# Performance work log

Measured on AMD Instinct MI355X. Metric: run time of the kernel, lower is better.

## Reference

```python
import jax, jax.numpy as jnp
import numpy as np

N = 10000       # nodes (= number of eigenpairs)
NFEAT = 512
NCLASS = 64     # hidden size of attention/FFN when norm='none'
HID = 128       # feat_encoder hidden
DIM = 32        # eig encoder hidden_dim
K = 10          # outer loop count of ParamNonHarmonicEncoding
NF = DIM // 2   # num_freq = 16
OMEGA = 50.0
DMIN = 0.25
NLAYER = 1


def _ln(x, g, b, eps=1e-5):
    m = jnp.mean(x, axis=-1, keepdims=True)
    v = jnp.mean((x - m) ** 2, axis=-1, keepdims=True)
    return g * (x - m) / jnp.sqrt(v + eps) + b


def setup_inputs() -> dict:
    key = jax.random.key(0)
    ks = jax.random.split(key, 32)
    f32 = jnp.float32
    def w(k, shape, s=0.05):
        return jax.random.normal(k, shape, dtype=f32) * s
    inp = {
        "e": jax.random.uniform(ks[0], (N,), dtype=f32),
        "u": jax.random.normal(ks[1], (N, N), dtype=f32) / np.float32(np.sqrt(N)),
        "x": jax.random.normal(ks[2], (N, NFEAT), dtype=f32),
        # feat_encoder: Linear(nfeat,hid) -> ReLU -> Linear(hid,nclass)
        "fe_w1": w(ks[3], (NFEAT, HID)), "fe_b1": jnp.zeros((HID,), f32),
        "fe_w2": w(ks[4], (HID, NCLASS)), "fe_b2": jnp.zeros((NCLASS,), f32),
        # ParamNonHarmonicEncoding
        "freq_deltas": jax.random.uniform(ks[5], (NF,), dtype=f32) * 0.5,
        "freq_bias": jnp.zeros((), f32),
        "readout_w": w(ks[6], (K, 1 + 2 * NF), 0.1),
        "readout_b": jnp.zeros((K,), f32),
        "alpha_w": w(ks[7], (K, 1), 0.3),   # nn.Linear(k,1,bias=False)
        # mha pre-norm
        "mha_ln_g": jnp.ones((NCLASS,), f32), "mha_ln_b": jnp.zeros((NCLASS,), f32),
        # Diff attention (H=1, hidden=nclass)
        "wq1": w(ks[8], (NCLASS, NCLASS)), "bq1": jnp.zeros((NCLASS,), f32),
        "wk1": w(ks[9], (NCLASS, NCLASS)), "bk1": jnp.zeros((NCLASS,), f32),
        "wq2": w(ks[10], (NCLASS, NCLASS)), "bq2": jnp.zeros((NCLASS,), f32),
        "wk2": w(ks[11], (NCLASS, NCLASS)), "bk2": jnp.zeros((NCLASS,), f32),
        "wv": w(ks[12], (NCLASS, NCLASS)), "bv": jnp.zeros((NCLASS,), f32),
        "lq1": w(ks[13], (NCLASS,), 0.1), "lk1": w(ks[14], (NCLASS,), 0.1),
        "lq2": w(ks[15], (NCLASS,), 0.1), "lk2": w(ks[16], (NCLASS,), 0.1),
        "attn_ln_g": jnp.ones((NCLASS,), f32), "attn_ln_b": jnp.zeros((NCLASS,), f32),
        "out_w": w(ks[17], (NCLASS, NCLASS)), "out_b": jnp.zeros((NCLASS,), f32),
        # gating
        "gate_ln_g": jnp.ones((3 * NCLASS,), f32), "gate_ln_b": jnp.zeros((3 * NCLASS,), f32),
        "gate_w": w(ks[18], (3 * NCLASS, 3)), "gate_b": jnp.zeros((3,), f32),
        # FFN
        "ffn_ln_g": jnp.ones((NCLASS,), f32), "ffn_ln_b": jnp.zeros((NCLASS,), f32),
        "ffn_w1": w(ks[19], (NCLASS, NCLASS)), "ffn_b1": jnp.zeros((NCLASS,), f32),
        "ffn_w2": w(ks[20], (NCLASS, NCLASS)), "ffn_b2": jnp.zeros((NCLASS,), f32),
    }
    return inp


def reference(e, u, x, fe_w1, fe_b1, fe_w2, fe_b2,
              freq_deltas, freq_bias, readout_w, readout_b, alpha_w,
              mha_ln_g, mha_ln_b,
              wq1, bq1, wk1, bk1, wq2, bq2, wk2, bk2, wv, bv,
              lq1, lk1, lq2, lk2, attn_ln_g, attn_ln_b, out_w, out_b,
              gate_ln_g, gate_ln_b, gate_w, gate_b,
              ffn_ln_g, ffn_ln_b, ffn_w1, ffn_b1, ffn_w2, ffn_b2):
    # feat encoder (all dropouts are 0 / eval mode)
    h = jnp.maximum(x @ fe_w1 + fe_b1, 0.0) @ fe_w2 + fe_b2          # [N, C]

    # ParamNonHarmonicEncoding, vectorized over the k powers
    deltas = jax.nn.softplus(freq_deltas) + DMIN
    freqs = jnp.cumsum(deltas) + freq_bias
    freqs = OMEGA * jnp.tanh(freqs / OMEGA)                           # [F]
    powers = e[:, None] ** jnp.arange(1, K + 1, dtype=e.dtype)        # [N, K]
    phase = powers[:, :, None] * freqs                                # [N, K, F]
    ns = jnp.asarray(NF ** 0.5, e.dtype)
    feat = jnp.concatenate(
        [jnp.ones_like(powers)[..., None], jnp.sin(phase) / ns, jnp.cos(phase) / ns],
        axis=-1)                                                      # [N, K, 1+2F]
    eig = jnp.einsum('nkf,kf->nk', feat, readout_w) + readout_b      # [N, K]
    new_e = eig @ alpha_w                                             # [N, 1]

    for layer in range(NLAYER):
        # spectral propagation: u @ diag-like(new_e) @ u^T @ h
        utx = u.T @ h                                                 # [N, C]
        h_fur = u @ (new_e * utx)                                     # [N, C]

        # differential linear attention
        mh = _ln(h, mha_ln_g, mha_ln_b)
        q1 = mh @ wq1 + bq1; k1 = mh @ wk1 + bk1
        q2 = mh @ wq2 + bq2; k2 = mh @ wk2 + bk2
        v = mh @ wv + bv
        k1v = k1.T @ v                                                # [C, C]
        k2v = k2.T @ v
        lam1 = jnp.exp(jnp.sum(lq1 * lk1))
        lam2 = jnp.exp(jnp.sum(lq2 * lk2))
        lam_init = 0.8 - 0.6 * float(np.exp(-0.3 * layer))
        lam_full = lam1 - lam2 + lam_init
        xa = q1 @ k1v - (q2 @ k2v) * lam_full
        xa = _ln(xa, attn_ln_g, attn_ln_b) * (1.0 - lam_init)
        mha_h = xa @ out_w + out_b                                    # [N, C]

        # gated mixing
        cat = jnp.concatenate([h, mha_h, h_fur], axis=-1)             # [N, 3C]
        g = jax.nn.softmax(_ln(cat, gate_ln_g, gate_ln_b) @ gate_w + gate_b, axis=-1)
        mix = h * g[:, 0:1] + mha_h * g[:, 1:2] + h_fur * g[:, 2:3]

        f = _ln(mix, ffn_ln_g, ffn_ln_b)
        f = jax.nn.gelu(f @ ffn_w1 + ffn_b1, approximate=False) @ ffn_w2 + ffn_b2
        h = mix + f
    return h
```

## Files before the change

kernel.cpp:

```cpp
#include <hip/hip_runtime.h>
#include <hip/hip_bf16.h>
#include <math.h>

#define NN 10000
#define J48 10048
#define CHUNKS 157
#define CPS 10
#define SPLITS 16

typedef __bf16 bf16;
typedef bf16 bf16x8 __attribute__((ext_vector_type(8)));
typedef float f32x4 __attribute__((ext_vector_type(4)));

__device__ __forceinline__ float wave_sum64(float v) {
#pragma unroll
  for (int m = 32; m >= 1; m >>= 1) v += __shfl_xor(v, m, 64);
  return v;
}

__global__ void prep_kernel(const float* __restrict__ w1, const float* __restrict__ w2,
                            const float* __restrict__ wq1, const float* __restrict__ wk1,
                            const float* __restrict__ wq2, const float* __restrict__ wk2,
                            const float* __restrict__ wvw,
                            const float* __restrict__ bq1, const float* __restrict__ bk1,
                            const float* __restrict__ bq2, const float* __restrict__ bk2,
                            const float* __restrict__ bvv,
                            const float* __restrict__ lq1, const float* __restrict__ lk1,
                            const float* __restrict__ lq2, const float* __restrict__ lk2,
                            const float* __restrict__ freq_deltas, const float* __restrict__ freq_bias,
                            bf16* __restrict__ w1T, bf16* __restrict__ w2T, bf16* __restrict__ qkvT,
                            float* __restrict__ bqkv, float* __restrict__ freqs, float* __restrict__ lamb) {
  int tid = blockIdx.x * blockDim.x + threadIdx.x;
  int nthr = gridDim.x * blockDim.x;
  for (int i = tid; i < 512 * 128; i += nthr) {
    int o = i >> 9, k = i & 511;
    w1T[i] = (bf16)w1[k * 128 + o];
  }
  for (int i = tid; i < 64 * 128; i += nthr) {
    int o = i >> 7, k = i & 127;
    w2T[i] = (bf16)w2[k * 64 + o];
  }
  for (int i = tid; i < 320 * 64; i += nthr) {
    int r = i >> 6, k = i & 63;
    const float* W = (r < 64) ? wq1 : (r < 128) ? wk1 : (r < 192) ? wq2 : (r < 256) ? wk2 : wvw;
    qkvT[i] = (bf16)W[k * 64 + (r & 63)];
  }
  for (int i = tid; i < 320; i += nthr) {
    const float* B = (i < 64) ? bq1 : (i < 128) ? bk1 : (i < 192) ? bq2 : (i < 256) ? bk2 : bvv;
    bqkv[i] = B[i & 63];
  }
  if (blockIdx.x == 0) {
    if (threadIdx.x == 0) {
      float acc = freq_bias[0];
      for (int f = 0; f < 16; f++) {
        acc += log1pf(expf(freq_deltas[f])) + 0.25f;
        freqs[f] = 50.0f * tanhf(acc * (1.0f / 50.0f));
      }
    }
    if (threadIdx.x >= 64 && threadIdx.x < 128) {
      int l = threadIdx.x - 64;
      float s1 = wave_sum64(lq1[l] * lk1[l]);
      float s2 = wave_sum64(lq2[l] * lk2[l]);
      if (l == 0) lamb[0] = expf(s1) - expf(s2) + 0.2f;
    }
  }
}

__global__ void newe_kernel(const float* __restrict__ e, const float* __restrict__ rw,
                            const float* __restrict__ rb, const float* __restrict__ aw,
                            const float* __restrict__ freqs, float* __restrict__ newe) {
  int n = blockIdx.x * blockDim.x + threadIdx.x;
  if (n >= NN) return;
  float fr[16];
#pragma unroll
  for (int f = 0; f < 16; f++) fr[f] = freqs[f];
  float ev = e[n], p = 1.0f, acc = 0.0f;
  for (int k = 0; k < 10; k++) {
    p *= ev;
    float s = rb[k] + rw[k * 33];
#pragma unroll
    for (int f = 0; f < 16; f++) {
      float ph = p * fr[f];
      s += 0.25f * (__sinf(ph) * rw[k * 33 + 1 + f] + __cosf(ph) * rw[k * 33 + 17 + f]);
    }
    acc += s * aw[k];
  }
  newe[n] = acc;
}

__global__ __launch_bounds__(256) void g1_kernel(const float* __restrict__ x, const bf16* __restrict__ w1T,
                                                 const float* __restrict__ b1, bf16* __restrict__ t1b) {
  __shared__ bf16 la[64][40];
  __shared__ bf16 lb[128][40];
  const int bm = blockIdx.x * 64;
  const int lane = threadIdx.x & 63, wvid = threadIdx.x >> 6;
  const int am = threadIdx.x >> 2, aseg = (threadIdx.x & 3) * 8;
  const int arow = bm + am;
  f32x4 acc[8] = {};
  float4 aLo, aHi;
  uint4 bChunk[2];
  auto fetchAll = [&](int k0) {
    if (arow < NN) {
      const float4* p = (const float4*)(x + (size_t)arow * 512 + k0 + aseg);
      aLo = p[0]; aHi = p[1];
    } else {
      aLo = make_float4(0.f, 0.f, 0.f, 0.f); aHi = aLo;
    }
#pragma unroll
    for (int r = 0; r < 2; r++) {
      int slot = threadIdx.x * 2 + r;
      int n = slot >> 2, seg = (slot & 3) * 8;
      bChunk[r] = *(const uint4*)(w1T + n * 512 + k0 + seg);
    }
  };
  auto store = [&]() {
    union { uint4 v; bf16 b[8]; } pk;
    float av[8] = {aLo.x, aLo.y, aLo.z, aLo.w, aHi.x, aHi.y, aHi.z, aHi.w};
#pragma unroll
    for (int t = 0; t < 8; t++) pk.b[t] = (bf16)av[t];
    *(uint4*)&la[am][aseg] = pk.v;
#pragma unroll
    for (int r = 0; r < 2; r++) {
      int slot = threadIdx.x * 2 + r;
      int n = slot >> 2, seg = (slot & 3) * 8;
      *(uint4*)&lb[n][seg] = bChunk[r];
    }
  };
  fetchAll(0);
  for (int k0 = 0; k0 < 512; k0 += 32) {
    store();
    if (k0 + 32 < 512) fetchAll(k0 + 32);
    __syncthreads();
    bf16x8 af = *(const bf16x8*)&la[wvid * 16 + (lane & 15)][(lane >> 4) * 8];
#pragma unroll
    for (int s = 0; s < 8; s++) {
      bf16x8 bfr = *(const bf16x8*)&lb[s * 16 + (lane & 15)][(lane >> 4) * 8];
      acc[s] = __builtin_amdgcn_mfma_f32_16x16x32_bf16(af, bfr, acc[s], 0, 0, 0);
    }
    __syncthreads();
  }
#pragma unroll
  for (int s = 0; s < 8; s++) {
    int col = s * 16 + (lane & 15);
    float bvv = b1[col];
#pragma unroll
    for (int r = 0; r < 4; r++) {
      int row = bm + wvid * 16 + (lane >> 4) * 4 + r;
      if (row < NN) {
        float v = acc[s][r] + bvv;
        t1b[(size_t)row * 128 + col] = (bf16)(v > 0.f ? v : 0.f);
      }
    }
  }
}

__global__ __launch_bounds__(256) void g2_kernel(const bf16* __restrict__ t1b, const bf16* __restrict__ w2T,
                                                 const float* __restrict__ b2, float* __restrict__ h,
                                                 bf16* __restrict__ hT) {
  __shared__ bf16 la[64][72];
  __shared__ bf16 lb[64][72];
  const int bm = blockIdx.x * 64;
  const int lane = threadIdx.x & 63, wvid = threadIdx.x >> 6;
  f32x4 acc[4] = {};
  for (int k0 = 0; k0 < 128; k0 += 64) {
#pragma unroll
    for (int r = 0; r < 2; r++) {
      int slot = threadIdx.x * 2 + r;
      int m = slot >> 3, seg = (slot & 7) * 8;
      int row = bm + m;
      uint4 val = make_uint4(0u, 0u, 0u, 0u);
      if (row < NN) val = *(const uint4*)(t1b + (size_t)row * 128 + k0 + seg);
      *(uint4*)&la[m][seg] = val;
      *(uint4*)&lb[m][seg] = *(const uint4*)(w2T + m * 128 + k0 + seg);
    }
    __syncthreads();
#pragma unroll
    for (int ks = 0; ks < 2; ks++) {
      bf16x8 af = *(const bf16x8*)&la[wvid * 16 + (lane & 15)][ks * 32 + (lane >> 4) * 8];
#pragma unroll
      for (int s = 0; s < 4; s++) {
        bf16x8 bfr = *(const bf16x8*)&lb[s * 16 + (lane & 15)][ks * 32 + (lane >> 4) * 8];
        acc[s] = __builtin_amdgcn_mfma_f32_16x16x32_bf16(af, bfr, acc[s], 0, 0, 0);
      }
    }
    __syncthreads();
  }
#pragma unroll
  for (int s = 0; s < 4; s++) {
    int col = s * 16 + (lane & 15);
    float bvv = b2[col];
#pragma unroll
    for (int r = 0; r < 4; r++) {
      int row = bm + wvid * 16 + (lane >> 4) * 4 + r;
      if (row < NN) {
        float v = acc[s][r] + bvv;
        h[(size_t)row * 64 + col] = v;
        hT[(size_t)col * NN + row] = (bf16)v;
      }
    }
  }
}

__global__ __launch_bounds__(256) void mhln_kernel(const float* __restrict__ h, const float* __restrict__ g,
                                                   const float* __restrict__ b, bf16* __restrict__ mh) {
  int row = blockIdx.x * 4 + (threadIdx.x >> 6);
  int lane = threadIdx.x & 63;
  if (row >= NN) return;
  float v = h[(size_t)row * 64 + lane];
  float m = wave_sum64(v) * (1.0f / 64.0f);
  float d = v - m;
  float var = wave_sum64(d * d) * (1.0f / 64.0f);
  mh[(size_t)row * 64 + lane] = (bf16)(g[lane] * d * rsqrtf(var + 1e-5f) + b[lane]);
}

__global__ __launch_bounds__(256) void qkv_kernel(const bf16* __restrict__ mh, const bf16* __restrict__ qkvT,
                                                  const float* __restrict__ bqkv,
                                                  bf16* __restrict__ qq, bf16* __restrict__ kv) {
  __shared__ bf16 la[64][72];
  __shared__ bf16 lb[320][72];
  const int bm = blockIdx.x * 64;
  const int lane = threadIdx.x & 63, wvid = threadIdx.x >> 6;
#pragma unroll
  for (int r = 0; r < 2; r++) {
    int slot = threadIdx.x * 2 + r;
    int m = slot >> 3, seg = (slot & 7) * 8;
    int row = bm + m;
    uint4 val = make_uint4(0u, 0u, 0u, 0u);
    if (row < NN) val = *(const uint4*)(mh + (size_t)row * 64 + seg);
    *(uint4*)&la[m][seg] = val;
  }
#pragma unroll
  for (int r = 0; r < 10; r++) {
    int slot = threadIdx.x * 10 + r;
    int n = slot >> 3, seg = (slot & 7) * 8;
    *(uint4*)&lb[n][seg] = *(const uint4*)(qkvT + n * 64 + seg);
  }
  __syncthreads();
  f32x4 acc[20] = {};
#pragma unroll
  for (int ks = 0; ks < 2; ks++) {
    bf16x8 af = *(const bf16x8*)&la[wvid * 16 + (lane & 15)][ks * 32 + (lane >> 4) * 8];
#pragma unroll
    for (int s = 0; s < 20; s++) {
      bf16x8 bfr = *(const bf16x8*)&lb[s * 16 + (lane & 15)][ks * 32 + (lane >> 4) * 8];
      acc[s] = __builtin_amdgcn_mfma_f32_16x16x32_bf16(af, bfr, acc[s], 0, 0, 0);
    }
  }
#pragma unroll
  for (int s = 0; s < 20; s++) {
    int col = s * 16 + (lane & 15);
    float bvv = bqkv[col];
    bf16* dst; int dc, stride;
    if (col < 64)       { dst = qq; dc = col;       stride = 128; }
    else if (col < 128) { dst = kv; dc = col - 64;  stride = 192; }
    else if (col < 192) { dst = qq; dc = col - 64;  stride = 128; }
    else                { dst = kv; dc = col - 128; stride = 192; }
#pragma unroll
    for (int r = 0; r < 4; r++) {
      int row = bm + wvid * 16 + (lane >> 4) * 4 + r;
      if (row < NN) dst[(size_t)row * stride + dc] = (bf16)(acc[s][r] + bvv);
    }
  }
}

__global__ __launch_bounds__(256) void r1_kernel(const bf16* __restrict__ kv, float* __restrict__ part) {
  int b = blockIdx.x;
  int c1 = threadIdx.x & 63, grp = threadIdx.x >> 6;
  int r0 = b * 40;
  float a1[16] = {}, a2[16] = {};
  for (int r = 0; r < 40; r++) {
    const bf16* rowp = kv + (size_t)(r0 + r) * 192;
    float k1 = (float)rowp[c1];
    float k2 = (float)rowp[64 + c1];
#pragma unroll
    for (int q = 0; q < 16; q++) {
      float vv = (float)rowp[128 + grp * 16 + q];
      a1[q] += k1 * vv; a2[q] += k2 * vv;
    }
  }
  float* p1 = part + ((size_t)(b * 2 + 0) * 64 + c1) * 64 + grp * 16;
  float* p2 = part + ((size_t)(b * 2 + 1) * 64 + c1) * 64 + grp * 16;
#pragma unroll
  for (int q = 0; q < 16; q++) { p1[q] = a1[q]; p2[q] = a2[q]; }
}

__global__ __launch_bounds__(256) void r2a_kernel(const float* __restrict__ part, float* __restrict__ part2) {
  int flat = blockIdx.x * 256 + threadIdx.x;
  int y = blockIdx.y;
  int b0 = y * 32, b1 = min(250, b0 + 32);
  float s = 0.f;
  for (int b = b0; b < b1; b++) s += part[(size_t)b * 8192 + flat];
  part2[(size_t)flat * 8 + y] = s;
}

__global__ void r2b_kernel(const float* __restrict__ part2, const float* __restrict__ lamb, bf16* __restrict__ Bt) {
  int flat = blockIdx.x * 256 + threadIdx.x;
  int mat = flat >> 12, rem = flat & 4095;
  int d = rem >> 6, c = rem & 63;
  f32x4 lo = *(const f32x4*)(part2 + (size_t)flat * 8);
  f32x4 hi = *(const f32x4*)(part2 + (size_t)flat * 8 + 4);
  float s = lo[0] + lo[1] + lo[2] + lo[3] + hi[0] + hi[1] + hi[2] + hi[3];
  float v = mat ? (-lamb[0] * s) : s;
  Bt[c * 128 + mat * 64 + d] = (bf16)v;
}

__global__ __launch_bounds__(256) void d_split_kernel(const float* __restrict__ u, const bf16* __restrict__ hT,
                                                      float* __restrict__ dpart) {
  __shared__ bf16 la[64][72];
  __shared__ bf16 lb[64][72];
  const int j0 = blockIdx.x * 64;
  const int sk = blockIdx.y;
  const int c0 = sk * CPS, c1e = min(CHUNKS, c0 + CPS);
  const int t = threadIdx.x;
  const int lane = t & 63, wv = t >> 6;
  const int jl = (t & 15) * 4;
  const int ir = (t >> 4) * 4;
  f32x4 acc[4] = {};
  uint4 aC[2];
  float4 bC[4];
  auto fetchAll = [&](int i0) {
#pragma unroll
    for (int r = 0; r < 2; r++) {
      int slot = t * 2 + r;
      int c = slot >> 3, seg = (slot & 7) * 8;
      int i = i0 + seg;
      if (i + 7 < NN) aC[r] = *(const uint4*)(hT + (size_t)c * NN + i);
      else {
        union { uint4 v; bf16 b[8]; } tu;
#pragma unroll
        for (int q = 0; q < 8; q++) tu.b[q] = (i + q < NN) ? hT[(size_t)c * NN + i + q] : (bf16)0.f;
        aC[r] = tu.v;
      }
    }
#pragma unroll
    for (int q = 0; q < 4; q++) {
      int i = i0 + ir + q;
      if (i < NN && (j0 + jl + 3) < NN) bC[q] = *(const float4*)(u + (size_t)i * NN + j0 + jl);
      else if (i < NN) {
        float tmp[4];
#pragma unroll
        for (int q2 = 0; q2 < 4; q2++) tmp[q2] = (j0 + jl + q2 < NN) ? u[(size_t)i * NN + j0 + jl + q2] : 0.f;
        bC[q] = make_float4(tmp[0], tmp[1], tmp[2], tmp[3]);
      } else bC[q] = make_float4(0.f, 0.f, 0.f, 0.f);
    }
  };
  auto storeAll = [&]() {
#pragma unroll
    for (int r = 0; r < 2; r++) {
      int slot = t * 2 + r;
      int c = slot >> 3, seg = (slot & 7) * 8;
      *(uint4*)&la[c][seg] = aC[r];
    }
#pragma unroll
    for (int q2 = 0; q2 < 4; q2++) {
      int j = jl + q2;
      int isw = ir ^ (((j >> 2) & 3) << 3);
      union { uint2 w; bf16 b[4]; } pk;
      pk.b[0] = (bf16)((float*)&bC[0])[q2];
      pk.b[1] = (bf16)((float*)&bC[1])[q2];
      pk.b[2] = (bf16)((float*)&bC[2])[q2];
      pk.b[3] = (bf16)((float*)&bC[3])[q2];
      *(uint2*)&lb[j][isw] = pk.w;
    }
  };
  fetchAll(c0 * 64);
  for (int ch = c0; ch < c1e; ch++) {
    storeAll();
    if (ch + 1 < c1e) fetchAll((ch + 1) * 64);
    __syncthreads();
#pragma unroll
    for (int ks = 0; ks < 2; ks++) {
      bf16x8 af = *(const bf16x8*)&la[wv * 16 + (lane & 15)][ks * 32 + (lane >> 4) * 8];
#pragma unroll
      for (int s = 0; s < 4; s++) {
        int j = s * 16 + (lane & 15);
        int ioff = (ks * 32 + (lane >> 4) * 8) ^ (((j >> 2) & 3) << 3);
        bf16x8 bfr = *(const bf16x8*)&lb[j][ioff];
        acc[s] = __builtin_amdgcn_mfma_f32_16x16x32_bf16(af, bfr, acc[s], 0, 0, 0);
      }
    }
    __syncthreads();
  }
#pragma unroll
  for (int s = 0; s < 4; s++) {
    int col = s * 16 + (lane & 15);
#pragma unroll
    for (int r = 0; r < 4; r++) {
      int c = wv * 16 + (lane >> 4) * 4 + r;
      dpart[((size_t)sk * 64 + c) * J48 + j0 + col] = acc[s][r];
    }
  }
}

__global__ void dred_kernel(const float* __restrict__ dpart, const float* __restrict__ newe,
                            bf16* __restrict__ wutxT) {
  int idx = blockIdx.x * 256 + threadIdx.x;
  int c = idx / 2512;
  int j = (idx - c * 2512) * 4;
  if (c >= 64 || j >= NN) return;
  f32x4 s = {};
  for (int sk = 0; sk < SPLITS; sk++)
    s += *(const f32x4*)(dpart + ((size_t)sk * 64 + c) * J48 + j);
  union { uint2 w; bf16 b[4]; } pk;
#pragma unroll
  for (int q = 0; q < 4; q++) pk.b[q] = (bf16)(newe[j + q] * s[q]);
  *(uint2*)&wutxT[(size_t)c * NN + j] = pk.w;
}

__global__ __launch_bounds__(256) void e_split_kernel(const float* __restrict__ u, const bf16* __restrict__ wutxT,
                                                      float* __restrict__ epart) {
  __shared__ bf16 la[64][72];
  __shared__ bf16 lb[64][72];
  const int bm = blockIdx.x * 64;
  const int sk = blockIdx.y;
  const int c0 = sk * CPS, c1e = min(CHUNKS, c0 + CPS);
  const int t = threadIdx.x;
  const int lane = t & 63, wv = t >> 6;
  const int mA = t >> 2, segA = (t & 3) * 16;
  const int mrow = bm + mA;
  f32x4 acc[4] = {};
  float4 aC[4];
  uint4 bC[2];
  auto fetchAll = [&](int j0) {
    int j = j0 + segA;
    if (mrow < NN && j + 15 < NN) {
      const float4* p = (const float4*)(u + (size_t)mrow * NN + j);
      aC[0] = p[0]; aC[1] = p[1]; aC[2] = p[2]; aC[3] = p[3];
    } else {
#pragma unroll
      for (int q = 0; q < 4; q++) {
        float tmp[4];
#pragma unroll
        for (int q2 = 0; q2 < 4; q2++) {
          int jj = j + q * 4 + q2;
          tmp[q2] = (mrow < NN && jj < NN) ? u[(size_t)mrow * NN + jj] : 0.f;
        }
        aC[q] = make_float4(tmp[0], tmp[1], tmp[2], tmp[3]);
      }
    }
#pragma unroll
    for (int r = 0; r < 2; r++) {
      int slot = t * 2 + r;
      int c = slot >> 3, seg = (slot & 7) * 8;
      int jj = j0 + seg;
      if (jj + 7 < NN) bC[r] = *(const uint4*)(wutxT + (size_t)c * NN + jj);
      else {
        union { uint4 v; bf16 b[8]; } tu;
#pragma unroll
        for (int q = 0; q < 8; q++) tu.b[q] = (jj + q < NN) ? wutxT[(size_t)c * NN + jj + q] : (bf16)0.f;
        bC[r] = tu.v;
      }
    }
  };
  auto storeAll = [&]() {
    union { uint4 v[2]; bf16 b[16]; } pk;
#pragma unroll
    for (int q = 0; q < 4; q++)
#pragma unroll
      for (int q2 = 0; q2 < 4; q2++) pk.b[q * 4 + q2] = (bf16)((float*)&aC[q])[q2];
    *(uint4*)&la[mA][segA] = pk.v[0];
    *(uint4*)&la[mA][segA + 8] = pk.v[1];
#pragma unroll
    for (int r = 0; r < 2; r++) {
      int slot = t * 2 + r;
      int c = slot >> 3, seg = (slot & 7) * 8;
      *(uint4*)&lb[c][seg] = bC[r];
    }
  };
  fetchAll(c0 * 64);
  for (int ch = c0; ch < c1e; ch++) {
    storeAll();
    if (ch + 1 < c1e) fetchAll((ch + 1) * 64);
    __syncthreads();
#pragma unroll
    for (int ks = 0; ks < 2; ks++) {
      bf16x8 af = *(const bf16x8*)&la[wv * 16 + (lane & 15)][ks * 32 + (lane >> 4) * 8];
#pragma unroll
      for (int s = 0; s < 4; s++) {
        bf16x8 bfr = *(const bf16x8*)&lb[s * 16 + (lane & 15)][ks * 32 + (lane >> 4) * 8];
        acc[s] = __builtin_amdgcn_mfma_f32_16x16x32_bf16(af, bfr, acc[s], 0, 0, 0);
      }
    }
    __syncthreads();
  }
#pragma unroll
  for (int s = 0; s < 4; s++) {
    int col = s * 16 + (lane & 15);
#pragma unroll
    for (int r = 0; r < 4; r++) {
      int row = wv * 16 + (lane >> 4) * 4 + r;
      epart[((size_t)sk * J48 + bm + row) * 64 + col] = acc[s][r];
    }
  }
}

__global__ void ered_kernel(const float* __restrict__ epart, float* __restrict__ h_fur) {
  int idx = blockIdx.x * 256 + threadIdx.x;
  if (idx >= NN * 16) return;
  size_t off = (size_t)idx * 4;
  f32x4 s = {};
  for (int sk = 0; sk < SPLITS; sk++)
    s += *(const f32x4*)(epart + (size_t)sk * (J48 * 64) + off);
  *(f32x4*)(h_fur + off) = s;
}

__global__ __launch_bounds__(256) void hattn_kernel(const bf16* __restrict__ qq, const bf16* __restrict__ Bt,
                                                    const float* __restrict__ g, const float* __restrict__ b,
                                                    bf16* __restrict__ xan) {
  __shared__ bf16 la[64][136];
  __shared__ bf16 lb[64][136];
  const int bm = blockIdx.x * 64;
  const int lane = threadIdx.x & 63, wvid = threadIdx.x >> 6;
#pragma unroll
  for (int r = 0; r < 4; r++) {
    int slot = threadIdx.x * 4 + r;
    int m = slot >> 4, seg = (slot & 15) * 8;
    int row = bm + m;
    uint4 val = make_uint4(0u, 0u, 0u, 0u);
    if (row < NN) val = *(const uint4*)(qq + (size_t)row * 128 + seg);
    *(uint4*)&la[m][seg] = val;
    *(uint4*)&lb[m][seg] = *(const uint4*)(Bt + m * 128 + seg);
  }
  __syncthreads();
  f32x4 acc[4] = {};
#pragma unroll
  for (int ks = 0; ks < 4; ks++) {
    bf16x8 af = *(const bf16x8*)&la[wvid * 16 + (lane & 15)][ks * 32 + (lane >> 4) * 8];
#pragma unroll
    for (int s = 0; s < 4; s++) {
      bf16x8 bfr = *(const bf16x8*)&lb[s * 16 + (lane & 15)][ks * 32 + (lane >> 4) * 8];
      acc[s] = __builtin_amdgcn_mfma_f32_16x16x32_bf16(af, bfr, acc[s], 0, 0, 0);
    }
  }
#pragma unroll
  for (int r = 0; r < 4; r++) {
    float psum = acc[0][r] + acc[1][r] + acc[2][r] + acc[3][r];
#pragma unroll
    for (int msk = 1; msk < 16; msk <<= 1) psum += __shfl_xor(psum, msk, 64);
    float mean = psum * (1.0f / 64.0f);
    float pvar = 0.f;
#pragma unroll
    for (int s = 0; s < 4; s++) { float dd = acc[s][r] - mean; pvar += dd * dd; }
#pragma unroll
    for (int msk = 1; msk < 16; msk <<= 1) pvar += __shfl_xor(pvar, msk, 64);
    float rsq = rsqrtf(pvar * (1.0f / 64.0f) + 1e-5f);
    int row = bm + wvid * 16 + (lane >> 4) * 4 + r;
    if (row < NN) {
#pragma unroll
      for (int s = 0; s < 4; s++) {
        int col = s * 16 + (lane & 15);
        float o = 0.8f * (g[col] * (acc[s][r] - mean) * rsq + b[col]);
        xan[(size_t)row * 64 + col] = (bf16)o;
      }
    }
  }
}

__global__ __launch_bounds__(256) void final_kernel(const float* __restrict__ h, const float* __restrict__ h_fur,
                                                    const bf16* __restrict__ xan,
                                                    const float* __restrict__ out_w, const float* __restrict__ out_b,
                                                    const float* __restrict__ gg, const float* __restrict__ gb,
                                                    const float* __restrict__ gw, const float* __restrict__ gbias,
                                                    const float* __restrict__ fg, const float* __restrict__ fb,
                                                    const float* __restrict__ fw1, const float* __restrict__ fb1,
                                                    const float* __restrict__ fw2, const float* __restrict__ fb2,
                                                    float* __restrict__ out) {
  __shared__ float s_ow[64][64];
  __shared__ float s_w1[64][64];
  __shared__ float s_w2[64][64];
  __shared__ float s_gw[192][3];
  __shared__ float s_row[4][64];
  const int lane = threadIdx.x & 63, wvid = threadIdx.x >> 6;
  for (int i = threadIdx.x; i < 4096; i += 256) {
    ((float*)s_ow)[i] = out_w[i];
    ((float*)s_w1)[i] = fw1[i];
    ((float*)s_w2)[i] = fw2[i];
  }
  for (int i = threadIdx.x; i < 576; i += 256) ((float*)s_gw)[i] = gw[i];
  const int row = blockIdx.x * 4 + wvid;
  float x_h = h[(size_t)row * 64 + lane];
  float x_f = h_fur[(size_t)row * 64 + lane];
  float x_a = (float)xan[(size_t)row * 64 + lane];
  s_row[wvid][lane] = x_a;
  __syncthreads();
  float mha = out_b[lane];
#pragma unroll 8
  for (int d = 0; d < 64; d++) mha += s_row[wvid][d] * s_ow[d][lane];
  float m3 = wave_sum64(x_h + mha + x_f) * (1.0f / 192.0f);
  float dh = x_h - m3, dm = mha - m3, df = x_f - m3;
  float v3 = wave_sum64(dh * dh + dm * dm + df * df) * (1.0f / 192.0f);
  float rs3 = rsqrtf(v3 + 1e-5f);
  float l0 = gg[lane] * dh * rs3 + gb[lane];
  float l1 = gg[64 + lane] * dm * rs3 + gb[64 + lane];
  float l2 = gg[128 + lane] * df * rs3 + gb[128 + lane];
  float p0 = l0 * s_gw[lane][0] + l1 * s_gw[64 + lane][0] + l2 * s_gw[128 + lane][0];
  float p1 = l0 * s_gw[lane][1] + l1 * s_gw[64 + lane][1] + l2 * s_gw[128 + lane][1];
  float p2 = l0 * s_gw[lane][2] + l1 * s_gw[64 + lane][2] + l2 * s_gw[128 + lane][2];
  p0 = wave_sum64(p0) + gbias[0];
  p1 = wave_sum64(p1) + gbias[1];
  p2 = wave_sum64(p2) + gbias[2];
  float mx = fmaxf(p0, fmaxf(p1, p2));
  float e0 = expf(p0 - mx), e1 = expf(p1 - mx), e2 = expf(p2 - mx);
  float inv = 1.0f / (e0 + e1 + e2);
  float mix = x_h * (e0 * inv) + mha * (e1 * inv) + x_f * (e2 * inv);
  float mf = wave_sum64(mix) * (1.0f / 64.0f);
  float dmx = mix - mf;
  float vf = wave_sum64(dmx * dmx) * (1.0f / 64.0f);
  float f = fg[lane] * dmx * rsqrtf(vf + 1e-5f) + fb[lane];
  __syncthreads();
  s_row[wvid][lane] = f;
  __syncthreads();
  float t1 = fb1[lane];
#pragma unroll 8
  for (int d = 0; d < 64; d++) t1 += s_row[wvid][d] * s_w1[d][lane];
  t1 = 0.5f * t1 * (1.0f + erff(t1 * 0.70710678118654752f));
  __syncthreads();
  s_row[wvid][lane] = t1;
  __syncthreads();
  float f2 = fb2[lane];
#pragma unroll 8
  for (int d = 0; d < 64; d++) f2 += s_row[wvid][d] * s_w2[d][lane];
  out[(size_t)row * 64 + lane] = mix + f2;
}

extern "C" void kernel_launch(void* const* d_in, const int* in_sizes, int n_in,
                              void* d_out, int out_size, void* d_ws, size_t ws_size,
                              hipStream_t stream) {
  const float* e          = (const float*)d_in[0];
  const float* u          = (const float*)d_in[1];
  const float* x          = (const float*)d_in[2];
  const float* fe_w1      = (const float*)d_in[3];
  const float* fe_b1      = (const float*)d_in[4];
  const float* fe_w2      = (const float*)d_in[5];
  const float* fe_b2      = (const float*)d_in[6];
  const float* freq_deltas= (const float*)d_in[7];
  const float* freq_bias  = (const float*)d_in[8];
  const float* readout_w  = (const float*)d_in[9];
  const float* readout_b  = (const float*)d_in[10];
  const float* alpha_w    = (const float*)d_in[11];
  const float* mha_ln_g   = (const float*)d_in[12];
  const float* mha_ln_b   = (const float*)d_in[13];
  const float* wq1        = (const float*)d_in[14];
  const float* bq1        = (const float*)d_in[15];
  const float* wk1        = (const float*)d_in[16];
  const float* bk1        = (const float*)d_in[17];
  const float* wq2        = (const float*)d_in[18];
  const float* bq2        = (const float*)d_in[19];
  const float* wk2        = (const float*)d_in[20];
  const float* bk2        = (const float*)d_in[21];
  const float* wv_in      = (const float*)d_in[22];
  const float* bv_in      = (const float*)d_in[23];
  const float* lq1        = (const float*)d_in[24];
  const float* lk1        = (const float*)d_in[25];
  const float* lq2        = (const float*)d_in[26];
  const float* lk2        = (const float*)d_in[27];
  const float* attn_ln_g  = (const float*)d_in[28];
  const float* attn_ln_b  = (const float*)d_in[29];
  const float* out_w      = (const float*)d_in[30];
  const float* out_b      = (const float*)d_in[31];
  const float* gate_ln_g  = (const float*)d_in[32];
  const float* gate_ln_b  = (const float*)d_in[33];
  const float* gate_w     = (const float*)d_in[34];
  const float* gate_b     = (const float*)d_in[35];
  const float* ffn_ln_g   = (const float*)d_in[36];
  const float* ffn_ln_b   = (const float*)d_in[37];
  const float* ffn_w1     = (const float*)d_in[38];
  const float* ffn_b1     = (const float*)d_in[39];
  const float* ffn_w2     = (const float*)d_in[40];
  const float* ffn_b2     = (const float*)d_in[41];

  constexpr size_t OFF_H     = 0;
  constexpr size_t OFF_T1B   = 2560000;
  constexpr size_t OFF_HT    = 5120000;
  constexpr size_t OFF_MH    = 6400000;
  constexpr size_t OFF_QQ    = 7680000;
  constexpr size_t OFF_KV    = 10240000;
  constexpr size_t OFF_WUTXT = 14080000;
  constexpr size_t OFF_HFUR  = 15360000;
  constexpr size_t OFF_XAN   = 17920000;
  constexpr size_t OFF_NEWE  = 19200000;
  constexpr size_t OFF_BT    = 19240064;
  constexpr size_t OFF_W1T   = 19256448;
  constexpr size_t OFF_W2T   = 19387520;
  constexpr size_t OFF_QKVT  = 19403904;
  constexpr size_t OFF_BQKV  = 19444864;
  constexpr size_t OFF_FREQS = 19446144;
  constexpr size_t OFF_LAM   = 19446208;
  constexpr size_t OFF_BIG   = 19446272;
  constexpr size_t OFF_PART2 = OFF_BIG + 8192000;
  constexpr size_t WS_NEED   = OFF_BIG + (size_t)SPLITS * J48 * 64 * 4;
  if (ws_size < WS_NEED) return;

  char* ws = (char*)d_ws;
  float* h_buf   = (float*)(ws + OFF_H);
  bf16*  t1b     = (bf16*)(ws + OFF_T1B);
  bf16*  hT      = (bf16*)(ws + OFF_HT);
  bf16*  mh      = (bf16*)(ws + OFF_MH);
  bf16*  qq      = (bf16*)(ws + OFF_QQ);
  bf16*  kv      = (bf16*)(ws + OFF_KV);
  bf16*  wutxT   = (bf16*)(ws + OFF_WUTXT);
  float* h_fur   = (float*)(ws + OFF_HFUR);
  bf16*  xan     = (bf16*)(ws + OFF_XAN);
  float* newe    = (float*)(ws + OFF_NEWE);
  bf16*  Bt      = (bf16*)(ws + OFF_BT);
  bf16*  w1T     = (bf16*)(ws + OFF_W1T);
  bf16*  w2T     = (bf16*)(ws + OFF_W2T);
  bf16*  qkvT    = (bf16*)(ws + OFF_QKVT);
  float* bqkv    = (float*)(ws + OFF_BQKV);
  float* freqs   = (float*)(ws + OFF_FREQS);
  float* lamb    = (float*)(ws + OFF_LAM);
  float* part    = (float*)(ws + OFF_BIG);
  float* part2   = (float*)(ws + OFF_PART2);
  float* spart   = (float*)(ws + OFF_BIG);

  prep_kernel<<<64, 256, 0, stream>>>(fe_w1, fe_w2, wq1, wk1, wq2, wk2, wv_in,
                                      bq1, bk1, bq2, bk2, bv_in,
                                      lq1, lk1, lq2, lk2, freq_deltas, freq_bias,
                                      w1T, w2T, qkvT, bqkv, freqs, lamb);
  newe_kernel<<<40, 256, 0, stream>>>(e, readout_w, readout_b, alpha_w, freqs, newe);
  g1_kernel<<<157, 256, 0, stream>>>(x, w1T, fe_b1, t1b);
  g2_kernel<<<157, 256, 0, stream>>>(t1b, w2T, fe_b2, h_buf, hT);
  mhln_kernel<<<2500, 256, 0, stream>>>(h_buf, mha_ln_g, mha_ln_b, mh);
  qkv_kernel<<<157, 256, 0, stream>>>(mh, qkvT, bqkv, qq, kv);
  r1_kernel<<<250, 256, 0, stream>>>(kv, part);
  r2a_kernel<<<dim3(32, 8), 256, 0, stream>>>(part, part2);
  r2b_kernel<<<32, 256, 0, stream>>>(part2, lamb, Bt);
  d_split_kernel<<<dim3(157, SPLITS), 256, 0, stream>>>(u, hT, spart);
  dred_kernel<<<628, 256, 0, stream>>>(spart, newe, wutxT);
  e_split_kernel<<<dim3(157, SPLITS), 256, 0, stream>>>(u, wutxT, spart);
  ered_kernel<<<625, 256, 0, stream>>>(spart, h_fur);
  hattn_kernel<<<157, 256, 0, stream>>>(qq, Bt, attn_ln_g, attn_ln_b, xan);
  final_kernel<<<2500, 256, 0, stream>>>(h_buf, h_fur, xan, out_w, out_b,
                                         gate_ln_g, gate_ln_b, gate_w, gate_b,
                                         ffn_ln_g, ffn_ln_b, ffn_w1, ffn_b1, ffn_w2, ffn_b2,
                                         (float*)d_out);
}
```

Measured before the change: 366.2 us.

## Pre-convert eigenvector matrix to bf16, fuse pre-norm LayerNorm into g2, retune splits

Adds a kernel that converts the 10000x10000 fp32 eigenvector matrix to bf16 once per call. Both spectral GEMMs (d_split and e_split) then stream half-size bf16 tiles and skip per-tile fp32-to-bf16 conversion. The aim is to cut the bytes those two large GEMMs read, at the cost of an extra full read of the fp32 matrix plus a 200MB bf16 write. It also fuses the MHA pre-LayerNorm into the g2 epilogue, which removes the mhln kernel. Other changes: r1 gets vectorized loads over more, smaller blocks, and the K-split count drops from 16 to 8 with twice as many chunks per split.

```diff
diff --git a/kernel.cpp b/kernel.cpp
--- a/kernel.cpp
+++ b/kernel.cpp
@@ -5,8 +5,8 @@
 #define NN 10000
 #define J48 10048
 #define CHUNKS 157
-#define CPS 10
-#define SPLITS 16
+#define CPS 20
+#define SPLITS 8
 
 typedef __bf16 bf16;
 typedef bf16 bf16x8 __attribute__((ext_vector_type(8)));
@@ -88,6 +88,19 @@
   newe[n] = acc;
 }
 
+__global__ __launch_bounds__(256) void ucopy_kernel(const float* __restrict__ u, bf16* __restrict__ ubf) {
+  size_t base = ((size_t)blockIdx.x * 256 + threadIdx.x) * 8;
+  size_t stride = (size_t)gridDim.x * 256 * 8;
+  for (size_t i = base; i < (size_t)NN * NN; i += stride) {
+    float4 a = *(const float4*)(u + i);
+    float4 b = *(const float4*)(u + i + 4);
+    union { uint4 v; bf16 h[8]; } pk;
+    pk.h[0] = (bf16)a.x; pk.h[1] = (bf16)a.y; pk.h[2] = (bf16)a.z; pk.h[3] = (bf16)a.w;
+    pk.h[4] = (bf16)b.x; pk.h[5] = (bf16)b.y; pk.h[6] = (bf16)b.z; pk.h[7] = (bf16)b.w;
+    *(uint4*)(ubf + i) = pk.v;
+  }
+}
+
 __global__ __launch_bounds__(256) void g1_kernel(const float* __restrict__ x, const bf16* __restrict__ w1T,
                                                  const float* __restrict__ b1, bf16* __restrict__ t1b) {
   __shared__ bf16 la[64][40];
@@ -155,8 +168,9 @@
 }
 
 __global__ __launch_bounds__(256) void g2_kernel(const bf16* __restrict__ t1b, const bf16* __restrict__ w2T,
-                                                 const float* __restrict__ b2, float* __restrict__ h,
-                                                 bf16* __restrict__ hT) {
+                                                 const float* __restrict__ b2, const float* __restrict__ lng,
+                                                 const float* __restrict__ lnb, float* __restrict__ h,
+                                                 bf16* __restrict__ hT, bf16* __restrict__ mh) {
   __shared__ bf16 la[64][72];
   __shared__ bf16 lb[64][72];
   const int bm = blockIdx.x * 64;
@@ -185,32 +199,38 @@
     }
     __syncthreads();
   }
+  float bv4[4], g4[4], lb4[4];
 #pragma unroll
   for (int s = 0; s < 4; s++) {
     int col = s * 16 + (lane & 15);
-    float bvv = b2[col];
-#pragma unroll
-    for (int r = 0; r < 4; r++) {
-      int row = bm + wvid * 16 + (lane >> 4) * 4 + r;
-      if (row < NN) {
-        float v = acc[s][r] + bvv;
+    bv4[s] = b2[col]; g4[s] = lng[col]; lb4[s] = lnb[col];
+  }
+#pragma unroll
+  for (int r = 0; r < 4; r++) {
+    float vals[4], psum = 0.f;
+#pragma unroll
+    for (int s = 0; s < 4; s++) { vals[s] = acc[s][r] + bv4[s]; psum += vals[s]; }
+#pragma unroll
+    for (int msk = 1; msk < 16; msk <<= 1) psum += __shfl_xor(psum, msk, 64);
+    float mean = psum * (1.0f / 64.0f);
+    float pvar = 0.f;
+#pragma unroll
+    for (int s = 0; s < 4; s++) { float dd = vals[s] - mean; pvar += dd * dd; }
+#pragma unroll
+    for (int msk = 1; msk < 16; msk <<= 1) pvar += __shfl_xor(pvar, msk, 64);
+    float rsq = rsqrtf(pvar * (1.0f / 64.0f) + 1e-5f);
+    int row = bm + wvid * 16 + (lane >> 4) * 4 + r;
+    if (row < NN) {
+#pragma unroll
+      for (int s = 0; s < 4; s++) {
+        int col = s * 16 + (lane & 15);
+        float v = vals[s];
         h[(size_t)row * 64 + col] = v;
         hT[(size_t)col * NN + row] = (bf16)v;
-      }
-    }
-  }
-}
-
-__global__ __launch_bounds__(256) void mhln_kernel(const float* __restrict__ h, const float* __restrict__ g,
-                                                   const float* __restrict__ b, bf16* __restrict__ mh) {
-  int row = blockIdx.x * 4 + (threadIdx.x >> 6);
-  int lane = threadIdx.x & 63;
-  if (row >= NN) return;
-  float v = h[(size_t)row * 64 + lane];
-  float m = wave_sum64(v) * (1.0f / 64.0f);
-  float d = v - m;
-  float var = wave_sum64(d * d) * (1.0f / 64.0f);
-  mh[(size_t)row * 64 + lane] = (bf16)(g[lane] * d * rsqrtf(var + 1e-5f) + b[lane]);
+        mh[(size_t)row * 64 + col] = (bf16)(g4[s] * (v - mean) * rsq + lb4[s]);
+      }
+    }
+  }
 }
 
 __global__ __launch_bounds__(256) void qkv_kernel(const bf16* __restrict__ mh, const bf16* __restrict__ qkvT,
@@ -266,20 +286,24 @@
 __global__ __launch_bounds__(256) void r1_kernel(const bf16* __restrict__ kv, float* __restrict__ part) {
   int b = blockIdx.x;
   int c1 = threadIdx.x & 63, grp = threadIdx.x >> 6;
-  int r0 = b * 40;
+  int r0 = b * 16;
   float a1[16] = {}, a2[16] = {};
-  for (int r = 0; r < 40; r++) {
+  for (int r = 0; r < 16; r++) {
     const bf16* rowp = kv + (size_t)(r0 + r) * 192;
     float k1 = (float)rowp[c1];
     float k2 = (float)rowp[64 + c1];
-#pragma unroll
-    for (int q = 0; q < 16; q++) {
-      float vv = (float)rowp[128 + grp * 16 + q];
-      a1[q] += k1 * vv; a2[q] += k2 * vv;
-    }
-  }
-  float* p1 = part + ((size_t)(b * 2 + 0) * 64 + c1) * 64 + grp * 16;
-  float* p2 = part + ((size_t)(b * 2 + 1) * 64 + c1) * 64 + grp * 16;
+    union { uint4 v; bf16 b[8]; } v0, v1;
+    v0.v = *(const uint4*)(rowp + 128 + grp * 16);
+    v1.v = *(const uint4*)(rowp + 136 + grp * 16);
+#pragma unroll
+    for (int q = 0; q < 8; q++) {
+      float va = (float)v0.b[q], vb = (float)v1.b[q];
+      a1[q] += k1 * va; a2[q] += k2 * va;
+      a1[8 + q] += k1 * vb; a2[8 + q] += k2 * vb;
+    }
+  }
+  float* p1 = part + (size_t)b * 8192 + (size_t)c1 * 64 + grp * 16;
+  float* p2 = p1 + 4096;
 #pragma unroll
   for (int q = 0; q < 16; q++) { p1[q] = a1[q]; p2[q] = a2[q]; }
 }
@@ -287,7 +311,7 @@
 __global__ __launch_bounds__(256) void r2a_kernel(const float* __restrict__ part, float* __restrict__ part2) {
   int flat = blockIdx.x * 256 + threadIdx.x;
   int y = blockIdx.y;
-  int b0 = y * 32, b1 = min(250, b0 + 32);
+  int b0 = y * 79, b1 = min(625, b0 + 79);
   float s = 0.f;
   for (int b = b0; b < b1; b++) s += part[(size_t)b * 8192 + flat];
   part2[(size_t)flat * 8 + y] = s;
@@ -304,7 +328,7 @@
   Bt[c * 128 + mat * 64 + d] = (bf16)v;
 }
 
-__global__ __launch_bounds__(256) void d_split_kernel(const float* __restrict__ u, const bf16* __restrict__ hT,
+__global__ __launch_bounds__(256) void d_split_kernel(const bf16* __restrict__ ubf, const bf16* __restrict__ hT,
                                                       float* __restrict__ dpart) {
   __shared__ bf16 la[64][72];
   __shared__ bf16 lb[64][72];
@@ -317,7 +341,7 @@
   const int ir = (t >> 4) * 4;
   f32x4 acc[4] = {};
   uint4 aC[2];
-  float4 bC[4];
+  uint2 uc[4];
   auto fetchAll = [&](int i0) {
 #pragma unroll
     for (int r = 0; r < 2; r++) {
@@ -335,13 +359,13 @@
 #pragma unroll
     for (int q = 0; q < 4; q++) {
       int i = i0 + ir + q;
-      if (i < NN && (j0 + jl + 3) < NN) bC[q] = *(const float4*)(u + (size_t)i * NN + j0 + jl);
+      if (i < NN && (j0 + jl + 3) < NN) uc[q] = *(const uint2*)(ubf + (size_t)i * NN + j0 + jl);
       else if (i < NN) {
-        float tmp[4];
-#pragma unroll
-        for (int q2 = 0; q2 < 4; q2++) tmp[q2] = (j0 + jl + q2 < NN) ? u[(size_t)i * NN + j0 + jl + q2] : 0.f;
-        bC[q] = make_float4(tmp[0], tmp[1], tmp[2], tmp[3]);
-      } else bC[q] = make_float4(0.f, 0.f, 0.f, 0.f);
+        union { uint2 w; bf16 b[4]; } tu;
+#pragma unroll
+        for (int q2 = 0; q2 < 4; q2++) tu.b[q2] = (j0 + jl + q2 < NN) ? ubf[(size_t)i * NN + j0 + jl + q2] : (bf16)0.f;
+        uc[q] = tu.w;
+      } else uc[q] = make_uint2(0u, 0u);
     }
   };
   auto storeAll = [&]() {
@@ -356,10 +380,10 @@
       int j = jl + q2;
       int isw = ir ^ (((j >> 2) & 3) << 3);
       union { uint2 w; bf16 b[4]; } pk;
-      pk.b[0] = (bf16)((float*)&bC[0])[q2];
-      pk.b[1] = (bf16)((float*)&bC[1])[q2];
-      pk.b[2] = (bf16)((float*)&bC[2])[q2];
-      pk.b[3] = (bf16)((float*)&bC[3])[q2];
+      pk.b[0] = ((const bf16*)&uc[0])[q2];
+      pk.b[1] = ((const bf16*)&uc[1])[q2];
+      pk.b[2] = ((const bf16*)&uc[2])[q2];
+      pk.b[3] = ((const bf16*)&uc[3])[q2];
       *(uint2*)&lb[j][isw] = pk.w;
     }
   };
@@ -383,11 +407,11 @@
   }
 #pragma unroll
   for (int s = 0; s < 4; s++) {
-    int col = s * 16 + (lane & 15);
+    int j = j0 + s * 16 + (lane & 15);
 #pragma unroll
     for (int r = 0; r < 4; r++) {
       int c = wv * 16 + (lane >> 4) * 4 + r;
-      dpart[((size_t)sk * 64 + c) * J48 + j0 + col] = acc[s][r];
+      dpart[((size_t)sk * 64 + c) * J48 + j] = acc[s][r];
     }
   }
 }
@@ -407,7 +431,7 @@
   *(uint2*)&wutxT[(size_t)c * NN + j] = pk.w;
 }
 
-__global__ __launch_bounds__(256) void e_split_kernel(const float* __restrict__ u, const bf16* __restrict__ wutxT,
+__global__ __launch_bounds__(256) void e_split_kernel(const bf16* __restrict__ ubf, const bf16* __restrict__ wutxT,
                                                       float* __restrict__ epart) {
   __shared__ bf16 la[64][72];
   __shared__ bf16 lb[64][72];
@@ -419,24 +443,19 @@
   const int mA = t >> 2, segA = (t & 3) * 16;
   const int mrow = bm + mA;
   f32x4 acc[4] = {};
-  float4 aC[4];
+  uint4 aU[2];
   uint4 bC[2];
   auto fetchAll = [&](int j0) {
     int j = j0 + segA;
     if (mrow < NN && j + 15 < NN) {
-      const float4* p = (const float4*)(u + (size_t)mrow * NN + j);
-      aC[0] = p[0]; aC[1] = p[1]; aC[2] = p[2]; aC[3] = p[3];
+      aU[0] = *(const uint4*)(ubf + (size_t)mrow * NN + j);
+      aU[1] = *(const uint4*)(ubf + (size_t)mrow * NN + j + 8);
     } else {
-#pragma unroll
-      for (int q = 0; q < 4; q++) {
-        float tmp[4];
-#pragma unroll
-        for (int q2 = 0; q2 < 4; q2++) {
-          int jj = j + q * 4 + q2;
-          tmp[q2] = (mrow < NN && jj < NN) ? u[(size_t)mrow * NN + jj] : 0.f;
-        }
-        aC[q] = make_float4(tmp[0], tmp[1], tmp[2], tmp[3]);
-      }
+      union { uint4 v[2]; bf16 b[16]; } tu;
+#pragma unroll
+      for (int q = 0; q < 16; q++)
+        tu.b[q] = (mrow < NN && j + q < NN) ? ubf[(size_t)mrow * NN + j + q] : (bf16)0.f;
+      aU[0] = tu.v[0]; aU[1] = tu.v[1];
     }
 #pragma unroll
     for (int r = 0; r < 2; r++) {
@@ -453,13 +472,8 @@
     }
   };
   auto storeAll = [&]() {
-    union { uint4 v[2]; bf16 b[16]; } pk;
-#pragma unroll
-    for (int q = 0; q < 4; q++)
-#pragma unroll
-      for (int q2 = 0; q2 < 4; q2++) pk.b[q * 4 + q2] = (bf16)((float*)&aC[q])[q2];
-    *(uint4*)&la[mA][segA] = pk.v[0];
-    *(uint4*)&la[mA][segA + 8] = pk.v[1];
+    *(uint4*)&la[mA][segA] = aU[0];
+    *(uint4*)&la[mA][segA + 8] = aU[1];
 #pragma unroll
     for (int r = 0; r < 2; r++) {
       int slot = t * 2 + r;
@@ -687,8 +701,10 @@
   constexpr size_t OFF_FREQS = 19446144;
   constexpr size_t OFF_LAM   = 19446208;
   constexpr size_t OFF_BIG   = 19446272;
-  constexpr size_t OFF_PART2 = OFF_BIG + 8192000;
-  constexpr size_t WS_NEED   = OFF_BIG + (size_t)SPLITS * J48 * 64 * 4;
+  constexpr size_t SZ_SPART  = (size_t)SPLITS * 64 * J48 * 4;
+  constexpr size_t OFF_PART2 = OFF_BIG + SZ_SPART;
+  constexpr size_t OFF_UBF   = OFF_PART2 + 262144;
+  constexpr size_t WS_NEED   = OFF_UBF + (size_t)NN * NN * 2;
   if (ws_size < WS_NEED) return;
 
   char* ws = (char*)d_ws;
@@ -711,7 +727,9 @@
   float* lamb    = (float*)(ws + OFF_LAM);
   float* part    = (float*)(ws + OFF_BIG);
   float* part2   = (float*)(ws + OFF_PART2);
-  float* spart   = (float*)(ws + OFF_BIG);
+  float* dpart   = (float*)(ws + OFF_BIG);
+  float* epart   = (float*)(ws + OFF_BIG);
+  bf16*  ubf     = (bf16*)(ws + OFF_UBF);
 
   prep_kernel<<<64, 256, 0, stream>>>(fe_w1, fe_w2, wq1, wk1, wq2, wk2, wv_in,
                                       bq1, bk1, bq2, bk2, bv_in,
@@ -719,16 +737,16 @@
                                       w1T, w2T, qkvT, bqkv, freqs, lamb);
   newe_kernel<<<40, 256, 0, stream>>>(e, readout_w, readout_b, alpha_w, freqs, newe);
   g1_kernel<<<157, 256, 0, stream>>>(x, w1T, fe_b1, t1b);
-  g2_kernel<<<157, 256, 0, stream>>>(t1b, w2T, fe_b2, h_buf, hT);
-  mhln_kernel<<<2500, 256, 0, stream>>>(h_buf, mha_ln_g, mha_ln_b, mh);
+  g2_kernel<<<157, 256, 0, stream>>>(t1b, w2T, fe_b2, mha_ln_g, mha_ln_b, h_buf, hT, mh);
   qkv_kernel<<<157, 256, 0, stream>>>(mh, qkvT, bqkv, qq, kv);
-  r1_kernel<<<250, 256, 0, stream>>>(kv, part);
+  r1_kernel<<<625, 256, 0, stream>>>(kv, part);
   r2a_kernel<<<dim3(32, 8), 256, 0, stream>>>(part, part2);
   r2b_kernel<<<32, 256, 0, stream>>>(part2, lamb, Bt);
-  d_split_kernel<<<dim3(157, SPLITS), 256, 0, stream>>>(u, hT, spart);
-  dred_kernel<<<628, 256, 0, stream>>>(spart, newe, wutxT);
-  e_split_kernel<<<dim3(157, SPLITS), 256, 0, stream>>>(u, wutxT, spart);
-  ered_kernel<<<625, 256, 0, stream>>>(spart, h_fur);
+  ucopy_kernel<<<2048, 256, 0, stream>>>(u, ubf);
+  d_split_kernel<<<dim3(157, SPLITS), 256, 0, stream>>>(ubf, hT, dpart);
+  dred_kernel<<<628, 256, 0, stream>>>(dpart, newe, wutxT);
+  e_split_kernel<<<dim3(157, SPLITS), 256, 0, stream>>>(ubf, wutxT, epart);
+  ered_kernel<<<625, 256, 0, stream>>>(epart, h_fur);
   hattn_kernel<<<157, 256, 0, stream>>>(qq, Bt, attn_ln_g, attn_ln_b, xan);
   final_kernel<<<2500, 256, 0, stream>>>(h_buf, h_fur, xan, out_w, out_b,
                                          gate_ln_g, gate_ln_b, gate_w, gate_b,
```

Measured after the change: 405.5 us. +10.7%, slower.
